# Optimization experiments

Measured on AMD Instinct MI355X. Metric: run time of the kernel, lower is better.

## Reference

```python
import jax, jax.numpy as jnp
import numpy as np

N_NODES = 100000
N_EDGES = 1600000
IN_FEATS = 64
OUT_FEATS = 64
NEG_SLOPE = 0.2


def setup_inputs() -> dict:
    key = jax.random.key(0)
    ks = jax.random.split(key, 8)
    feat = jax.random.normal(ks[0], (N_NODES, IN_FEATS), dtype=jnp.float32)
    src = jax.random.randint(ks[1], (N_EDGES,), 0, N_NODES, dtype=jnp.int64 if jax.config.jax_enable_x64 else jnp.int32).astype(jnp.int32)
    dst = jax.random.randint(ks[2], (N_EDGES,), 0, N_NODES, dtype=jnp.int64 if jax.config.jax_enable_x64 else jnp.int32).astype(jnp.int32)
    scale = 1.0 / np.sqrt(IN_FEATS)
    Wq = jax.random.normal(ks[3], (IN_FEATS, OUT_FEATS), dtype=jnp.float32) * scale
    Wk = jax.random.normal(ks[4], (IN_FEATS, OUT_FEATS), dtype=jnp.float32) * scale
    Wf = jax.random.normal(ks[5], (IN_FEATS, OUT_FEATS), dtype=jnp.float32) * scale
    bq = jnp.zeros((OUT_FEATS,), dtype=jnp.float32)
    bk = jnp.zeros((OUT_FEATS,), dtype=jnp.float32)
    bf = jnp.zeros((OUT_FEATS,), dtype=jnp.float32)
    return {"feat": feat, "src": src, "dst": dst, "Wq": Wq, "bq": bq,
            "Wk": Wk, "bk": bk, "Wf": Wf, "bf": bf}


def reference(feat, src, dst, Wq, bq, Wk, bk, Wf, bf):
    N = feat.shape[0]
    # dense node projections (feat_drop=0 -> identity)
    q = feat @ Wq + bq          # [N, D] Query per destination node
    k = feat @ Wk + bk          # [N, D] Key per source node
    f = feat @ Wf + bf          # [N, D] message features
    # per-edge logit: u_dot_v(key, query)
    e = jnp.sum(k[src] * q[dst], axis=-1)              # [E]
    e = jax.nn.leaky_relu(e, negative_slope=NEG_SLOPE)
    # edge softmax grouped by destination node (numerically stable)
    emax = jax.ops.segment_max(e, dst, num_segments=N)  # [N]
    emax = jnp.where(jnp.isfinite(emax), emax, 0.0)     # empty segments -> 0
    ez = jnp.exp(e - emax[dst])                         # [E]
    denom = jax.ops.segment_sum(ez, dst, num_segments=N)  # [N]
    a = ez / denom[dst]                                  # [E] (attn_drop=0)
    # weighted scatter-sum aggregation: sum_e a_e * f[src_e] -> dst
    out = jax.ops.segment_sum(f[src] * a[:, None], dst, num_segments=N)  # [N, D]
    return out
```

## Files before the change

kernel.cpp:

```cpp
#include <hip/hip_runtime.h>
#include <math.h>

#define N_NODES   100000
#define N_EDGES   1600000
#define D         64
#define NEG_SLOPE 0.2f

#define SLOTS 56
#define ROW   64

#define NBUCK  64
#define BUCK_N 1563
#define BCAP   32768
#define CURS_STRIDE 16

typedef __attribute__((ext_vector_type(8))) _Float16 half8;
typedef __attribute__((ext_vector_type(2))) _Float16 half2v;
typedef __attribute__((ext_vector_type(4))) float floatx4;
typedef __attribute__((ext_vector_type(4))) int   intx4;

__device__ __forceinline__ unsigned short bfbits(float x) {
    unsigned u = __float_as_uint(x);
    u += 0x7fffu + ((u >> 16) & 1u);
    return (unsigned short)(u >> 16);
}
__device__ __forceinline__ float blo(unsigned v) { return __uint_as_float(v << 16); }
__device__ __forceinline__ float bhi(unsigned v) { return __uint_as_float(v & 0xffff0000u); }
__device__ __forceinline__ unsigned short h16(float x) {
    union { _Float16 h; unsigned short u; } c; c.h = (_Float16)x; return c.u;
}
__device__ __forceinline__ half2v u2h(unsigned v) {
    union { unsigned u; half2v h; } c; c.u = v; return c.h;
}
__device__ __forceinline__ float fdot2(unsigned a, half2v b, float c) {
#if __has_builtin(__builtin_amdgcn_fdot2)
    return __builtin_amdgcn_fdot2(u2h(a), b, c, false);
#else
    half2v ah = u2h(a);
    return c + (float)ah[0] * (float)b[0] + (float)ah[1] * (float)b[1];
#endif
}

#define WT_STRIDE 72
#define PROJ_BLOCKS 512
#define PROJ_WAVES  (PROJ_BLOCKS * 4)
#define PART_BLOCKS ((N_EDGES + 2047) / 2048)
#define FUSED_BLOCKS (PROJ_BLOCKS + PART_BLOCKS)

__global__ __launch_bounds__(256, 2) void proj_part_k(
    const float* __restrict__ feat,
    const float* __restrict__ Wq, const float* __restrict__ bq,
    const float* __restrict__ Wk, const float* __restrict__ bk,
    const float* __restrict__ Wf, const float* __restrict__ bf,
    unsigned short* __restrict__ qh, unsigned short* __restrict__ kf,
    const int* __restrict__ src, const int* __restrict__ dst,
    unsigned* __restrict__ bucketbuf, int* __restrict__ cursor) {

    const int bx  = blockIdx.x;
    const int tid = threadIdx.x;

    __shared__ int smi[3 * 64 * WT_STRIDE / 2];

    if (bx >= PROJ_BLOCKS) {
        const int hid = bx - PROJ_BLOCKS;
        int* lcnt  = smi;
        int* lbase = smi + NBUCK;
        if (tid < NBUCK) lcnt[tid] = 0;
        __syncthreads();

        int bkt[8]; int rnk[8]; unsigned pk[8];
        #pragma unroll
        for (int s2 = 0; s2 < 8; s2++) bkt[s2] = -1;

        const int cbase = hid * 2048;
        #pragma unroll
        for (int g = 0; g < 2; g++) {
            int eb = cbase + (g * 256 + tid) * 4;
            if (eb < N_EDGES) {
                intx4 d4 = __builtin_nontemporal_load((const intx4*)(dst + eb));
                intx4 s4 = __builtin_nontemporal_load((const intx4*)(src + eb));
                { int dd = d4.x, ss = s4.x; int b = dd / BUCK_N; bkt[g*4+0] = b;
                  rnk[g*4+0] = atomicAdd(&lcnt[b], 1);
                  pk[g*4+0]  = ((unsigned)ss << 11) | (unsigned)(dd - b * BUCK_N); }
                { int dd = d4.y, ss = s4.y; int b = dd / BUCK_N; bkt[g*4+1] = b;
                  rnk[g*4+1] = atomicAdd(&lcnt[b], 1);
                  pk[g*4+1]  = ((unsigned)ss << 11) | (unsigned)(dd - b * BUCK_N); }
                { int dd = d4.z, ss = s4.z; int b = dd / BUCK_N; bkt[g*4+2] = b;
                  rnk[g*4+2] = atomicAdd(&lcnt[b], 1);
                  pk[g*4+2]  = ((unsigned)ss << 11) | (unsigned)(dd - b * BUCK_N); }
                { int dd = d4.w, ss = s4.w; int b = dd / BUCK_N; bkt[g*4+3] = b;
                  rnk[g*4+3] = atomicAdd(&lcnt[b], 1);
                  pk[g*4+3]  = ((unsigned)ss << 11) | (unsigned)(dd - b * BUCK_N); }
            }
        }
        __syncthreads();
        if (tid < NBUCK)
            lbase[tid] = atomicAdd(&cursor[tid * CURS_STRIDE], lcnt[tid]);
        __syncthreads();
        #pragma unroll
        for (int s2 = 0; s2 < 8; s2++) {
            int b = bkt[s2];
            if (b >= 0) {
                int idx = lbase[b] + rnk[s2];
                if (idx < BCAP) bucketbuf[(size_t)b * BCAP + idx] = pk[s2];
            }
        }
        return;
    }

    const int pid  = bx;
    unsigned short* wt = (unsigned short*)smi;

    const int lane = tid & 63;
    const int wave = tid >> 6;
    const int m    = lane & 15;
    const int quad = lane >> 4;

    for (int idx = tid; idx < 64 * 64; idx += 256) {
        int i = idx >> 6, dd = idx & 63;
        int o = dd * WT_STRIDE + i;
        wt[0 * 64 * WT_STRIDE + o] = h16(Wq[idx]);
        wt[1 * 64 * WT_STRIDE + o] = h16(Wk[idx]);
        wt[2 * 64 * WT_STRIDE + o] = h16(Wf[idx]);
    }
    __syncthreads();

    half8 Bf[3][4][2];
    float bias[3][4];
    #pragma unroll
    for (int w = 0; w < 3; w++)
        #pragma unroll
        for (int nt = 0; nt < 4; nt++) {
            int n = nt * 16 + m;
            #pragma unroll
            for (int ks = 0; ks < 2; ks++)
                Bf[w][nt][ks] = *(const half8*)&wt[(w * 64 + n) * WT_STRIDE + ks * 32 + quad * 8];
        }
    #pragma unroll
    for (int nt = 0; nt < 4; nt++) {
        int n = nt * 16 + m;
        bias[0][nt] = bq[n]; bias[1][nt] = bk[n]; bias[2][nt] = bf[n];
    }

    const int NT  = N_NODES / 16;
    const int wid = pid * 4 + wave;

    for (int t = wid; t < NT; t += PROJ_WAVES) {
        int t0  = t * 16;
        int row = t0 + m;

        const floatx4* fr = (const floatx4*)(feat + (size_t)row * D + quad * 8);
        floatx4 x0 = __builtin_nontemporal_load(fr);
        floatx4 x1 = __builtin_nontemporal_load(fr + 1);
        floatx4 x2 = __builtin_nontemporal_load(fr + 8);
        floatx4 x3 = __builtin_nontemporal_load(fr + 9);

        half8 a0, a1;
        a0[0] = (_Float16)x0.x; a0[1] = (_Float16)x0.y;
        a0[2] = (_Float16)x0.z; a0[3] = (_Float16)x0.w;
        a0[4] = (_Float16)x1.x; a0[5] = (_Float16)x1.y;
        a0[6] = (_Float16)x1.z; a0[7] = (_Float16)x1.w;
        a1[0] = (_Float16)x2.x; a1[1] = (_Float16)x2.y;
        a1[2] = (_Float16)x2.z; a1[3] = (_Float16)x2.w;
        a1[4] = (_Float16)x3.x; a1[5] = (_Float16)x3.y;
        a1[6] = (_Float16)x3.z; a1[7] = (_Float16)x3.w;

        floatx4 acc[3][4];
        #pragma unroll
        for (int w = 0; w < 3; w++)
            #pragma unroll
            for (int nt = 0; nt < 4; nt++) {
                floatx4 c = {bias[w][nt], bias[w][nt], bias[w][nt], bias[w][nt]};
                c = __builtin_amdgcn_mfma_f32_16x16x32_f16(a0, Bf[w][nt][0], c, 0, 0, 0);
                c = __builtin_amdgcn_mfma_f32_16x16x32_f16(a1, Bf[w][nt][1], c, 0, 0, 0);
                acc[w][nt] = c;
            }

        #pragma unroll
        for (int nt = 0; nt < 4; nt++) {
            int dim = nt * 16 + m;
            #pragma unroll
            for (int r = 0; r < 4; r++) {
                int node = t0 + quad * 4 + r;
                __builtin_nontemporal_store(h16(acc[0][nt][r]),   qh + (size_t)node * D + dim);
                __builtin_nontemporal_store(h16(acc[1][nt][r]),   kf + (size_t)node * 128 + dim);
                __builtin_nontemporal_store(bfbits(acc[2][nt][r]), kf + (size_t)node * 128 + 64 + dim);
            }
        }
    }
}

__global__ __launch_bounds__(256) void build_k(
    const int* __restrict__ cursor, const unsigned* __restrict__ bucketbuf,
    int* __restrict__ srcperm, int* __restrict__ counts) {

    const int b = blockIdx.x;

    __shared__ int cnt[BUCK_N];
    for (int i = threadIdx.x; i < BUCK_N; i += 256) cnt[i] = 0;
    __syncthreads();

    int total = cursor[b * CURS_STRIDE];
    if (total > BCAP) total = BCAP;
    const unsigned* bb = bucketbuf + (size_t)b * BCAP;
    const int gbase = b * BUCK_N;

    #define TRYE(pp) {                                                        \
        int loc = (int)((pp) & 0x7FFu);                                       \
        int r = atomicAdd(&cnt[loc], 1);                                      \
        if (r < SLOTS)                                                        \
            srcperm[(size_t)(gbase + loc) * ROW + r] =                        \
                (int)((pp) >> 11) << 8;         \
    }

    int nv4 = total >> 2;
    for (int i = threadIdx.x; i < nv4; i += 256) {
        uint4 p4 = *(const uint4*)(bb + (size_t)i * 4);
        TRYE(p4.x) TRYE(p4.y) TRYE(p4.z) TRYE(p4.w)
    }
    if (threadIdx.x < (total & 3)) {
        unsigned pp = bb[(size_t)nv4 * 4 + threadIdx.x];
        TRYE(pp)
    }
    #undef TRYE
    __syncthreads();

    for (int i = threadIdx.x; i < BUCK_N; i += 256) {
        int node = gbase + i;
        if (node < N_NODES) counts[node] = cnt[i];
    }
}

__global__ __launch_bounds__(256) void node_agg_k(
    const int* __restrict__ counts, const int* __restrict__ srcperm,
    const unsigned short* __restrict__ qh, const unsigned short* __restrict__ kf,
    float* __restrict__ out) {

    int wave = threadIdx.x >> 6;
    int lane = threadIdx.x & 63;
    int n    = blockIdx.x * 4 + wave;
    if (n >= N_NODES) return;

    const int l8 = lane & 7;
    const int eg = lane >> 3;

    int offs_all = srcperm[(size_t)n * ROW + lane];
    uint4 uq = *(const uint4*)(qh + (size_t)n * D + l8 * 8);
    half2v qp0 = u2h(uq.x), qp1 = u2h(uq.y), qp2 = u2h(uq.z), qp3 = u2h(uq.w);

    int deg = counts[n];
    if (deg > SLOTS) deg = SLOTS;

    const char* kfb = (const char*)kf;

    float acc[8] = {0, 0, 0, 0, 0, 0, 0, 0};
    float l = 0.0f;

    bool v   = eg < deg;
    int  off = __shfl(offs_all, eg);
    off = v ? off : 0;
    uint4 ku = *(const uint4*)(kfb + off + l8 * 16);
    uint4 fu = *(const uint4*)(kfb + off + 128 + l8 * 16);

    for (int i0 = 0; i0 < deg; i0 += 8) {
        bool hasnext = (i0 + 8) < deg;
        int  i2  = i0 + 8 + eg;
        bool v2  = i2 < deg;
        int  off2 = __shfl(offs_all, i2);
        off2 = v2 ? off2 : 0;
        uint4 kn = ku, fn = fu;
        if (hasnext) {
            kn = *(const uint4*)(kfb + off2 + l8 * 16);
            fn = *(const uint4*)(kfb + off2 + 128 + l8 * 16);
        }

        float dot = 0.0f;
        dot = fdot2(ku.x, qp0, dot);
        dot = fdot2(ku.y, qp1, dot);
        dot = fdot2(ku.z, qp2, dot);
        dot = fdot2(ku.w, qp3, dot);
        dot += __shfl_xor(dot, 1);
        dot += __shfl_xor(dot, 2);
        dot += __shfl_xor(dot, 4);

        float e  = dot > 0.0f ? dot : NEG_SLOPE * dot;
        e = fminf(e, 85.0f);
        float ez = v ? __expf(e) : 0.0f;
        l += ez;

        acc[0] = fmaf(ez, blo(fu.x), acc[0]);
        acc[1] = fmaf(ez, bhi(fu.x), acc[1]);
        acc[2] = fmaf(ez, blo(fu.y), acc[2]);
        acc[3] = fmaf(ez, bhi(fu.y), acc[3]);
        acc[4] = fmaf(ez, blo(fu.z), acc[4]);
        acc[5] = fmaf(ez, bhi(fu.z), acc[5]);
        acc[6] = fmaf(ez, blo(fu.w), acc[6]);
        acc[7] = fmaf(ez, bhi(fu.w), acc[7]);

        ku = kn; fu = fn; v = v2;
    }

    #pragma unroll
    for (int d2 = 8; d2 < 64; d2 <<= 1) {
        #pragma unroll
        for (int j = 0; j < 8; j++) acc[j] += __shfl_xor(acc[j], d2);
    }
    #pragma unroll
    for (int d2 = 1; d2 < 64; d2 <<= 1) l += __shfl_xor(l, d2);

    float inv = (deg > 0) ? 8.0f / fmaxf(l, 1e-30f) : 0.0f;
    if (eg == 0) {
        floatx4 o0 = {acc[0] * inv, acc[1] * inv, acc[2] * inv, acc[3] * inv};
        floatx4 o1 = {acc[4] * inv, acc[5] * inv, acc[6] * inv, acc[7] * inv};
        floatx4* op = (floatx4*)(out + (size_t)n * D + l8 * 8);
        __builtin_nontemporal_store(o0, op);
        __builtin_nontemporal_store(o1, op + 1);
    }
}

extern "C" void kernel_launch(void* const* d_in, const int* in_sizes, int n_in,
                              void* d_out, int out_size, void* d_ws, size_t ws_size,
                              hipStream_t stream) {
    const float* feat = (const float*)d_in[0];
    const int*   src  = (const int*)d_in[1];
    const int*   dst  = (const int*)d_in[2];
    const float* Wq   = (const float*)d_in[3];
    const float* bq   = (const float*)d_in[4];
    const float* Wk   = (const float*)d_in[5];
    const float* bk   = (const float*)d_in[6];
    const float* Wf   = (const float*)d_in[7];
    const float* bf   = (const float*)d_in[8];
    float* out = (float*)d_out;

    unsigned short* qh      = (unsigned short*)d_ws;
    unsigned short* kf      = qh + (size_t)N_NODES * D;
    int*            srcperm = (int*)(kf + (size_t)N_NODES * 2 * D);
    int*            counts  = srcperm + (size_t)N_NODES * ROW;

    unsigned* bucketbuf = (unsigned*)d_out;
    int*      cursor    = (int*)d_out + (size_t)NBUCK * BCAP;

    hipMemsetAsync(cursor, 0, NBUCK * CURS_STRIDE * sizeof(int), stream);

    proj_part_k<<<FUSED_BLOCKS, 256, 0, stream>>>(
        feat, Wq, bq, Wk, bk, Wf, bf, qh, kf, src, dst, bucketbuf, cursor);

    build_k<<<NBUCK, 256, 0, stream>>>(cursor, bucketbuf, srcperm, counts);

    node_agg_k<<<(N_NODES + 3) / 4, 256, 0, stream>>>(counts, srcperm, qh, kf, out);
}
```

Before: 207.0 us.

## Run partition alone, then fuse bucket build with projection across 256 buckets

Edge partitioning now runs as its own kernel. The per-bucket CSR build is merged into the projection kernel so the build overlaps with the MFMA node projections, rather than running as a separate kernel after the projection. The bucket count grows from 64 to 256 with smaller per-bucket capacity, which gives the build phase more parallel blocks and shrinks the LDS counter array. Risks are bucket overflow at BCAP 8192 (mean about 6250 edges per bucket) and more contention on the global cursor atomics.

Result: no change. 204.9 us (-1.0%).

```diff
diff --git a/kernel.cpp b/kernel.cpp
--- a/kernel.cpp
+++ b/kernel.cpp
@@ -9,10 +9,12 @@
 #define SLOTS 56
 #define ROW   64
 
-#define NBUCK  64
-#define BUCK_N 1563
-#define BCAP   32768
+#define NBUCK  256
+#define BUCK_N 391
+#define BCAP   8192
 #define CURS_STRIDE 16
+#define PK_SHIFT 9
+#define PK_MASK  0x1FFu
 
 typedef __attribute__((ext_vector_type(8))) _Float16 half8;
 typedef __attribute__((ext_vector_type(2))) _Float16 half2v;
@@ -41,74 +43,117 @@
 #endif
 }
 
+#define PART_BLOCKS ((N_EDGES + 2047) / 2048)
+
+__global__ __launch_bounds__(256) void partition_k(
+    const int* __restrict__ src, const int* __restrict__ dst,
+    unsigned* __restrict__ bucketbuf, int* __restrict__ cursor) {
+
+    const int tid = threadIdx.x;
+    const int hid = blockIdx.x;
+
+    __shared__ int lcnt[NBUCK];
+    __shared__ int lbase[NBUCK];
+    lcnt[tid] = 0;
+    __syncthreads();
+
+    int bkt[8]; int rnk[8]; unsigned pk[8];
+    #pragma unroll
+    for (int s2 = 0; s2 < 8; s2++) bkt[s2] = -1;
+
+    const int cbase = hid * 2048;
+    #pragma unroll
+    for (int g = 0; g < 2; g++) {
+        int eb = cbase + (g * 256 + tid) * 4;
+        if (eb < N_EDGES) {
+            intx4 d4 = __builtin_nontemporal_load((const intx4*)(dst + eb));
+            intx4 s4 = __builtin_nontemporal_load((const intx4*)(src + eb));
+            { int dd = d4.x, ss = s4.x; int b = dd / BUCK_N; bkt[g*4+0] = b;
+              rnk[g*4+0] = atomicAdd(&lcnt[b], 1);
+              pk[g*4+0]  = ((unsigned)ss << PK_SHIFT) | (unsigned)(dd - b * BUCK_N); }
+            { int dd = d4.y, ss = s4.y; int b = dd / BUCK_N; bkt[g*4+1] = b;
+              rnk[g*4+1] = atomicAdd(&lcnt[b], 1);
+              pk[g*4+1]  = ((unsigned)ss << PK_SHIFT) | (unsigned)(dd - b * BUCK_N); }
+            { int dd = d4.z, ss = s4.z; int b = dd / BUCK_N; bkt[g*4+2] = b;
+              rnk[g*4+2] = atomicAdd(&lcnt[b], 1);
+              pk[g*4+2]  = ((unsigned)ss << PK_SHIFT) | (unsigned)(dd - b * BUCK_N); }
+            { int dd = d4.w, ss = s4.w; int b = dd / BUCK_N; bkt[g*4+3] = b;
+              rnk[g*4+3] = atomicAdd(&lcnt[b], 1);
+              pk[g*4+3]  = ((unsigned)ss << PK_SHIFT) | (unsigned)(dd - b * BUCK_N); }
+        }
+    }
+    __syncthreads();
+    lbase[tid] = atomicAdd(&cursor[tid * CURS_STRIDE], lcnt[tid]);
+    __syncthreads();
+    #pragma unroll
+    for (int s2 = 0; s2 < 8; s2++) {
+        int b = bkt[s2];
+        if (b >= 0) {
+            int idx = lbase[b] + rnk[s2];
+            if (idx < BCAP) bucketbuf[(size_t)b * BCAP + idx] = pk[s2];
+        }
+    }
+}
+
 #define WT_STRIDE 72
+#define BUILD_BLOCKS NBUCK
 #define PROJ_BLOCKS 512
 #define PROJ_WAVES  (PROJ_BLOCKS * 4)
-#define PART_BLOCKS ((N_EDGES + 2047) / 2048)
-#define FUSED_BLOCKS (PROJ_BLOCKS + PART_BLOCKS)
-
-__global__ __launch_bounds__(256, 2) void proj_part_k(
+#define FUSED_BLOCKS (BUILD_BLOCKS + PROJ_BLOCKS)
+
+__global__ __launch_bounds__(256, 2) void build_proj_k(
     const float* __restrict__ feat,
     const float* __restrict__ Wq, const float* __restrict__ bq,
     const float* __restrict__ Wk, const float* __restrict__ bk,
     const float* __restrict__ Wf, const float* __restrict__ bf,
     unsigned short* __restrict__ qh, unsigned short* __restrict__ kf,
-    const int* __restrict__ src, const int* __restrict__ dst,
-    unsigned* __restrict__ bucketbuf, int* __restrict__ cursor) {
+    const int* __restrict__ cursor, const unsigned* __restrict__ bucketbuf,
+    int* __restrict__ srcperm, int* __restrict__ counts) {
 
     const int bx  = blockIdx.x;
     const int tid = threadIdx.x;
 
     __shared__ int smi[3 * 64 * WT_STRIDE / 2];
 
-    if (bx >= PROJ_BLOCKS) {
-        const int hid = bx - PROJ_BLOCKS;
-        int* lcnt  = smi;
-        int* lbase = smi + NBUCK;
-        if (tid < NBUCK) lcnt[tid] = 0;
+    if (bx < BUILD_BLOCKS) {
+        const int b = bx;
+        int* cnt = smi;
+        for (int i = tid; i < BUCK_N; i += 256) cnt[i] = 0;
         __syncthreads();
 
-        int bkt[8]; int rnk[8]; unsigned pk[8];
-        #pragma unroll
-        for (int s2 = 0; s2 < 8; s2++) bkt[s2] = -1;
-
-        const int cbase = hid * 2048;
-        #pragma unroll
-        for (int g = 0; g < 2; g++) {
-            int eb = cbase + (g * 256 + tid) * 4;
-            if (eb < N_EDGES) {
-                intx4 d4 = __builtin_nontemporal_load((const intx4*)(dst + eb));
-                intx4 s4 = __builtin_nontemporal_load((const intx4*)(src + eb));
-                { int dd = d4.x, ss = s4.x; int b = dd / BUCK_N; bkt[g*4+0] = b;
-                  rnk[g*4+0] = atomicAdd(&lcnt[b], 1);
-                  pk[g*4+0]  = ((unsigned)ss << 11) | (unsigned)(dd - b * BUCK_N); }
-                { int dd = d4.y, ss = s4.y; int b = dd / BUCK_N; bkt[g*4+1] = b;
-                  rnk[g*4+1] = atomicAdd(&lcnt[b], 1);
-                  pk[g*4+1]  = ((unsigned)ss << 11) | (unsigned)(dd - b * BUCK_N); }
-                { int dd = d4.z, ss = s4.z; int b = dd / BUCK_N; bkt[g*4+2] = b;
-                  rnk[g*4+2] = atomicAdd(&lcnt[b], 1);
-                  pk[g*4+2]  = ((unsigned)ss << 11) | (unsigned)(dd - b * BUCK_N); }
-                { int dd = d4.w, ss = s4.w; int b = dd / BUCK_N; bkt[g*4+3] = b;
-                  rnk[g*4+3] = atomicAdd(&lcnt[b], 1);
-                  pk[g*4+3]  = ((unsigned)ss << 11) | (unsigned)(dd - b * BUCK_N); }
-            }
-        }
+        int total = cursor[b * CURS_STRIDE];
+        if (total > BCAP) total = BCAP;
+        const unsigned* bb = bucketbuf + (size_t)b * BCAP;
+        const int gbase = b * BUCK_N;
+
+        #define TRYE(pp) {                                                    \
+            int loc = (int)((pp) & PK_MASK);                                  \
+            int r = atomicAdd(&cnt[loc], 1);                                  \
+            if (r < SLOTS)                                                    \
+                srcperm[(size_t)(gbase + loc) * ROW + r] =                    \
+                    (int)((pp) >> PK_SHIFT) << 8;  \
+        }
+
+        int nv4 = total >> 2;
+        for (int i = tid; i < nv4; i += 256) {
+            uint4 p4 = *(const uint4*)(bb + (size_t)i * 4);
+            TRYE(p4.x) TRYE(p4.y) TRYE(p4.z) TRYE(p4.w)
+        }
+        if (tid < (total & 3)) {
+            unsigned pp = bb[(size_t)nv4 * 4 + tid];
+            TRYE(pp)
+        }
+        #undef TRYE
         __syncthreads();
-        if (tid < NBUCK)
-            lbase[tid] = atomicAdd(&cursor[tid * CURS_STRIDE], lcnt[tid]);
-        __syncthreads();
-        #pragma unroll
-        for (int s2 = 0; s2 < 8; s2++) {
-            int b = bkt[s2];
-            if (b >= 0) {
-                int idx = lbase[b] + rnk[s2];
-                if (idx < BCAP) bucketbuf[(size_t)b * BCAP + idx] = pk[s2];
-            }
+
+        for (int i = tid; i < BUCK_N; i += 256) {
+            int node = gbase + i;
+            if (node < N_NODES) counts[node] = cnt[i];
         }
         return;
     }
 
-    const int pid  = bx;
+    const int pid  = bx - BUILD_BLOCKS;
     unsigned short* wt = (unsigned short*)smi;
 
     const int lane = tid & 63;
@@ -187,47 +232,6 @@
                 __builtin_nontemporal_store(bfbits(acc[2][nt][r]), kf + (size_t)node * 128 + 64 + dim);
             }
         }
-    }
-}
-
-__global__ __launch_bounds__(256) void build_k(
-    const int* __restrict__ cursor, const unsigned* __restrict__ bucketbuf,
-    int* __restrict__ srcperm, int* __restrict__ counts) {
-
-    const int b = blockIdx.x;
-
-    __shared__ int cnt[BUCK_N];
-    for (int i = threadIdx.x; i < BUCK_N; i += 256) cnt[i] = 0;
-    __syncthreads();
-
-    int total = cursor[b * CURS_STRIDE];
-    if (total > BCAP) total = BCAP;
-    const unsigned* bb = bucketbuf + (size_t)b * BCAP;
-    const int gbase = b * BUCK_N;
-
-    #define TRYE(pp) {                                                        \
-        int loc = (int)((pp) & 0x7FFu);                                       \
-        int r = atomicAdd(&cnt[loc], 1);                                      \
-        if (r < SLOTS)                                                        \
-            srcperm[(size_t)(gbase + loc) * ROW + r] =                        \
-                (int)((pp) >> 11) << 8;         \
-    }
-
-    int nv4 = total >> 2;
-    for (int i = threadIdx.x; i < nv4; i += 256) {
-        uint4 p4 = *(const uint4*)(bb + (size_t)i * 4);
-        TRYE(p4.x) TRYE(p4.y) TRYE(p4.z) TRYE(p4.w)
-    }
-    if (threadIdx.x < (total & 3)) {
-        unsigned pp = bb[(size_t)nv4 * 4 + threadIdx.x];
-        TRYE(pp)
-    }
-    #undef TRYE
-    __syncthreads();
-
-    for (int i = threadIdx.x; i < BUCK_N; i += 256) {
-        int node = gbase + i;
-        if (node < N_NODES) counts[node] = cnt[i];
     }
 }
 
@@ -342,10 +346,10 @@
 
     hipMemsetAsync(cursor, 0, NBUCK * CURS_STRIDE * sizeof(int), stream);
 
-    proj_part_k<<<FUSED_BLOCKS, 256, 0, stream>>>(
-        feat, Wq, bq, Wk, bk, Wf, bf, qh, kf, src, dst, bucketbuf, cursor);
-
-    build_k<<<NBUCK, 256, 0, stream>>>(cursor, bucketbuf, srcperm, counts);
+    partition_k<<<PART_BLOCKS, 256, 0, stream>>>(src, dst, bucketbuf, cursor);
+
+    build_proj_k<<<FUSED_BLOCKS, 256, 0, stream>>>(
+        feat, Wq, bq, Wk, bk, Wf, bf, qh, kf, cursor, bucketbuf, srcperm, counts);
 
     node_agg_k<<<(N_NODES + 3) / 4, 256, 0, stream>>>(counts, srcperm, qh, kf, out);
 }
```
